# Kernel optimization log

Hardware: AMD Instinct MI355X
Metric: run time of the kernel (lower is better)

## Reference

```python
import jax, jax.numpy as jnp
import numpy as np
from jax.scipy.linalg import expm

B, S, D = 8, 2048, 1024          # batch, seq, input_dim
C, CD = 16, 64                   # num_concepts, concept_dim
L = C * CD                       # latent_dim = 1024
ALPHA, BETA = 0.3, 1.0
LN_EPS = 1e-5                    # torch nn.LayerNorm default


def layer_norm(x, g, b):
    m = jnp.mean(x, axis=-1, keepdims=True)
    v = jnp.mean(jnp.square(x - m), axis=-1, keepdims=True)
    return (x - m) * jax.lax.rsqrt(v + LN_EPS) * g + b


def setup_inputs() -> dict:
    key = jax.random.key(0)
    ks = jax.random.split(key, 8)
    sc = 0.02
    return {
        "x": jax.random.normal(ks[0], (B, S, D), jnp.float32),
        # encoder: Linear(D, 2L) + LayerNorm(2L)
        "enc_w": jax.random.normal(ks[1], (2 * L, D), jnp.float32) * sc,
        "enc_b": jnp.zeros((2 * L,), jnp.float32),
        "enc_g": jnp.ones((2 * L,), jnp.float32),
        "enc_bt": jnp.zeros((2 * L,), jnp.float32),
        # DAG weights [C, C] (torch inits zeros; use small random for non-trivial math)
        "dag_w": jax.random.normal(ks[2], (C, C), jnp.float32) * 0.1,
        # per-concept transforms: Linear(CD,CD) -> LN(CD) -> ReLU -> Linear(CD,CD), stacked over C
        "cw1": jax.random.normal(ks[3], (C, CD, CD), jnp.float32) * sc,
        "cb1": jnp.zeros((C, CD), jnp.float32),
        "cg": jnp.ones((C, CD), jnp.float32),
        "cbt": jnp.zeros((C, CD), jnp.float32),
        "cw2": jax.random.normal(ks[4], (C, CD, CD), jnp.float32) * sc,
        "cb2": jnp.zeros((C, CD), jnp.float32),
        # decoder: Linear(L,L) -> LN(L) -> ReLU -> Linear(L,D)
        "dec_w1": jax.random.normal(ks[5], (L, L), jnp.float32) * sc,
        "dec_b1": jnp.zeros((L,), jnp.float32),
        "dec_g": jnp.ones((L,), jnp.float32),
        "dec_bt": jnp.zeros((L,), jnp.float32),
        "dec_w2": jax.random.normal(ks[6], (D, L), jnp.float32) * sc,
        "dec_b2": jnp.zeros((D,), jnp.float32),
    }


def reference(x, enc_w, enc_b, enc_g, enc_bt, dag_w, cw1, cb1, cg, cbt, cw2, cb2,
              dec_w1, dec_b1, dec_g, dec_bt, dec_w2, dec_b2):
    # ---- encode ----
    h = layer_norm(jnp.einsum('bsd,kd->bsk', x, enc_w) + enc_b, enc_g, enc_bt)  # [B,S,2L]
    mu, logvar = jnp.split(h, 2, axis=-1)                                        # [B,S,L] each
    z = mu  # eval-mode reparameterize

    # ---- causal transform ----
    zc = z.reshape(B, S, C, CD)                                   # [B,S,C,CD]
    dag = jnp.tril(jax.nn.softplus(dag_w), k=-1)                  # [C,C]
    z_causal = zc + jnp.einsum('ij,bsjd->bsid', dag, zc)          # [B,S,C,CD]

    # per-concept Linear -> LN -> ReLU -> Linear, batched over concept axis
    t = jnp.einsum('bsce,cde->bscd', z_causal, cw1) + cb1         # [B,S,C,CD]
    t = layer_norm(t, cg, cbt)
    t = jax.nn.relu(t)
    t = jnp.einsum('bsce,cde->bscd', t, cw2) + cb2
    z_t = t.reshape(B, S, L)

    # ---- decode ----
    d = layer_norm(jnp.einsum('bsl,kl->bsk', z_t, dec_w1) + dec_b1, dec_g, dec_bt)
    d = jax.nn.relu(d)
    x_recon = jnp.einsum('bsl,dl->bsd', d, dec_w2) + dec_b2        # [B,S,D]

    # ---- losses ----
    recon_loss = jnp.mean(jnp.square(x_recon - x))
    kl_loss = -0.5 * jnp.mean(1.0 + logvar - jnp.square(mu) - jnp.exp(logvar))
    dag_loss = jnp.sum(jnp.abs(dag)) + jnp.trace(expm(dag))
    total_loss = recon_loss + ALPHA * kl_loss + BETA * dag_loss
    return x_recon, total_loss, kl_loss, recon_loss, dag_loss
```

## Files before the change

### kernel.cpp

```cpp
#include <hip/hip_runtime.h>
#include <stdint.h>


#define NTOK   16384
#define DIM    1024
#define NC     16
#define CD     64
#define NOUT_ELEMS 16777216

typedef float f32x4 __attribute__((ext_vector_type(4)));
typedef __bf16 bf16x8 __attribute__((ext_vector_type(8)));
typedef unsigned short u16x4 __attribute__((ext_vector_type(4)));
typedef unsigned short u16x8 __attribute__((ext_vector_type(8)));

__device__ float g_scal[3];
__device__ float g_part[512];

__device__ __forceinline__ float b2f(uint16_t u) {
  union { uint32_t i; float f; } v; v.i = ((uint32_t)u) << 16; return v.f;
}
__device__ __forceinline__ uint16_t f2b(float f) {
  union { float f; uint32_t i; } v; v.f = f;
  uint32_t x = v.i;
  return (uint16_t)((x + 0x7fffu + ((x >> 16) & 1u)) >> 16);
}

__device__ __forceinline__ void gload_lds16(const uint16_t* g, uint16_t* l) {
  __builtin_amdgcn_global_load_lds(
      (const __attribute__((address_space(1))) void*)g,
      (__attribute__((address_space(3))) void*)l, 16, 0, 0);
}

__device__ __forceinline__ void cvt8(const float* s, uint16_t* d) {
  const f32x4 a = *(const f32x4*)s;
  const f32x4 b = *(const f32x4*)(s + 4);
  u16x8 o;
  o[0]=f2b(a[0]); o[1]=f2b(a[1]); o[2]=f2b(a[2]); o[3]=f2b(a[3]);
  o[4]=f2b(b[0]); o[5]=f2b(b[1]); o[6]=f2b(b[2]); o[7]=f2b(b[3]);
  *(u16x8*)d = o;
}

__global__ __launch_bounds__(256) void cvt_all_kernel(
    const float* __restrict__ x, uint16_t* __restrict__ xdst,
    const float* __restrict__ ew, const float* __restrict__ d1,
    const float* __restrict__ d2, const float* __restrict__ c1,
    const float* __restrict__ c2, uint16_t* __restrict__ out,
    const float* __restrict__ dag_w)
{
  const int blk = blockIdx.x;
  if (blk < 8192) {
    const int i = blk * 256 + threadIdx.x;
    cvt8(x + (size_t)i * 8, xdst + (size_t)i * 8);
    return;
  }
  if (blk == 10304) {
    const int t = threadIdx.x;
    g_part[t] = 0.f;
    g_part[256 + t] = 0.f;
    const int i2 = t >> 4, j2 = t & 15;
    const float v = (j2 < i2) ? log1pf(expf(dag_w[t])) : 0.f;
    float s = v;
#pragma unroll
    for (int m = 1; m < 64; m <<= 1) s += __shfl_xor(s, m);
    __shared__ float red[4];
    const int wave = t >> 6, lane = t & 63;
    if (lane == 0) red[wave] = s;
    __syncthreads();
    if (t == 0)
      g_scal[2] = red[0] + red[1] + red[2] + red[3] + 16.f;
    return;
  }
  const int i = (blk - 8192) * 256 + threadIdx.x;
  const float* src; uint16_t* dst; int off;
  if (i < 262144)      { src = ew; dst = out;           off = i; }
  else if (i < 393216) { src = d1; dst = out + 2097152; off = i - 262144; }
  else if (i < 524288) { src = d2; dst = out + 3145728; off = i - 393216; }
  else if (i < 532480) { src = c1; dst = out + 4194304; off = i - 524288; }
  else                 { src = c2; dst = out + 4259840; off = i - 532480; }
  cvt8(src + (size_t)off * 8, dst + (size_t)off * 8);
}

__device__ __forceinline__ void stage_half(
    const uint16_t* __restrict__ G, uint16_t* L, int h, int lda,
    int sr, int pc, int wave)
{
#pragma unroll
  for (int i = 0; i < 2; ++i) {
    const int r = h * 128 + i * 64 + sr;
    gload_lds16(G + (size_t)r * lda + (size_t)((pc ^ (sr & 7)) * 8),
                (uint16_t*)((char*)L + h * 16384 + i * 8192 + wave * 1024));
  }
}

template<typename TC, bool SPLIT, int RECON_MODE>
__global__ __launch_bounds__(512, 2) void gemm256_kernel(
    const uint16_t* __restrict__ A, const uint16_t* __restrict__ Wm,
    const float* __restrict__ bias, TC* __restrict__ C0, TC* __restrict__ C1,
    const void* __restrict__ Xref,
    int K, int lda, int ldw, int ldc)
{
  __shared__ __align__(16) uint16_t lds[65536];

  const int tid  = threadIdx.x;
  const int wave = tid >> 6;
  const int lane = tid & 63;
  const int q    = lane >> 4;
  const int r16  = lane & 15;
  const int wm   = wave >> 2;
  const int wn   = wave & 3;
  const int sr   = tid >> 3;
  const int pc   = tid & 7;

  const int gx  = gridDim.x;
  const int gy  = gridDim.y;
  const int nwg = gx * gy;
  const int o   = blockIdx.y * gx + blockIdx.x;
  const int w   = (o & 7) * (nwg >> 3) + (o >> 3);
  const int bn  = (w & (gy - 1)) * 256;
  const int bm  = (w >> __builtin_ctz(gy)) * 256;

  const uint16_t* Ab = A  + (size_t)bm * lda;
  const uint16_t* Wb = Wm + (size_t)bn * ldw;

  const int T = K >> 6;

  stage_half(Ab,      lds,                 0, lda, sr, pc, wave);
  stage_half(Ab,      lds,                 1, lda, sr, pc, wave);
  stage_half(Wb,      lds + 16384,         0, ldw, sr, pc, wave);
  stage_half(Wb,      lds + 16384,         1, ldw, sr, pc, wave);
  if (T > 1) {
    stage_half(Wb + 64, lds + 32768 + 16384, 0, ldw, sr, pc, wave);
    stage_half(Wb + 64, lds + 32768 + 16384, 1, ldw, sr, pc, wave);
    asm volatile("s_waitcnt vmcnt(4)" ::: "memory");
  } else {
    asm volatile("s_waitcnt vmcnt(0)" ::: "memory");
  }
  __builtin_amdgcn_s_barrier();

  f32x4 acc[8][4] = {};
  const int cxa = r16 & 7;
  const int c0  = (q ^ cxa) * 8;
  const int c1  = ((4 + q) ^ cxa) * 8;

  for (int t = 0; t < T; ++t) {
    uint16_t* As  = lds + (t & 1) * 32768;
    uint16_t* Bs  = As + 16384;
    uint16_t* Asn = lds + ((t & 1) ^ 1) * 32768;

    const uint16_t* a_rd = As + (wm * 128 + r16) * 64;
    const uint16_t* b_rd = Bs + (wn * 64  + r16) * 64;

    bf16x8 bfr[4][2];

#pragma unroll
    for (int p = 0; p < 4; ++p) {
      bf16x8 af[2][2];
#pragma unroll
      for (int mi2 = 0; mi2 < 2; ++mi2) {
        af[mi2][0] = *(const bf16x8*)(a_rd + (p * 2 + mi2) * 1024 + c0);
        af[mi2][1] = *(const bf16x8*)(a_rd + (p * 2 + mi2) * 1024 + c1);
      }
      if (p == 0) {
#pragma unroll
        for (int ni = 0; ni < 4; ++ni) {
          bfr[ni][0] = *(const bf16x8*)(b_rd + ni * 1024 + c0);
          bfr[ni][1] = *(const bf16x8*)(b_rd + ni * 1024 + c1);
        }
        if (t + 1 < T) {
          stage_half(Ab + (size_t)(t + 1) * 64, Asn, 0, lda, sr, pc, wave);
          stage_half(Ab + (size_t)(t + 1) * 64, Asn, 1, lda, sr, pc, wave);
        }
      } else if (p == 1) {
        if (t + 2 < T)
          stage_half(Wb + (size_t)(t + 2) * 64, Bs, 0, ldw, sr, pc, wave);
      } else if (p == 2) {
        if (t + 2 < T)
          stage_half(Wb + (size_t)(t + 2) * 64, Bs, 1, ldw, sr, pc, wave);
      }

      __builtin_amdgcn_s_barrier();
      __builtin_amdgcn_s_setprio(1);
#pragma unroll
      for (int ks = 0; ks < 2; ++ks)
#pragma unroll
        for (int mi2 = 0; mi2 < 2; ++mi2)
#pragma unroll
          for (int ni = 0; ni < 4; ++ni)
            acc[p * 2 + mi2][ni] = __builtin_amdgcn_mfma_f32_16x16x32_bf16(
                af[mi2][ks], bfr[ni][ks], acc[p * 2 + mi2][ni], 0, 0, 0);
      __builtin_amdgcn_s_setprio(0);
      if (p == 3) {
        if (t + 2 < T)      asm volatile("s_waitcnt vmcnt(4)" ::: "memory");
        else if (t + 1 < T) asm volatile("s_waitcnt vmcnt(0)" ::: "memory");
      }
      __builtin_amdgcn_s_barrier();
    }
  }

  TC* Cq = C0;
  int cb = bn;
  if constexpr (SPLIT) {
    if (bn >= 1024) { Cq = C1; cb = bn - 1024; }
  }
  float bv[4];
#pragma unroll
  for (int ni = 0; ni < 4; ++ni) bv[ni] = bias[bn + wn * 64 + ni * 16 + r16];

  float rsum = 0.f;
#pragma unroll
  for (int mi = 0; mi < 8; ++mi) {
    const int rbase = bm + wm * 128 + mi * 16 + q * 4;
#pragma unroll
    for (int r = 0; r < 4; ++r) {
      const size_t rowoff = (size_t)(rbase + r) * ldc + cb;
#pragma unroll
      for (int ni = 0; ni < 4; ++ni) {
        const int loc = wn * 64 + ni * 16 + r16;
        const float v = acc[mi][ni][r] + bv[ni];
        if constexpr (sizeof(TC) == 2)
          Cq[rowoff + loc] = f2b(v);
        else
          Cq[rowoff + loc] = v;
        if constexpr (RECON_MODE == 1) {
          const float dd = v - ((const float*)Xref)[rowoff + loc];
          rsum += dd * dd;
        } else if constexpr (RECON_MODE == 2) {
          const float dd = v - b2f(((const uint16_t*)Xref)[rowoff + loc]);
          rsum += dd * dd;
        }
      }
    }
  }
  if constexpr (RECON_MODE != 0) {
#pragma unroll
    for (int m = 1; m < 64; m <<= 1) rsum += __shfl_xor(rsum, m);
    __shared__ float redR[8];
    if (lane == 0) redR[wave] = rsum;
    __syncthreads();
    if (tid == 0) {
      float s = 0.f;
#pragma unroll
      for (int w2 = 0; w2 < 8; ++w2) s += redR[w2];
      atomicAdd(&g_part[256 + (w & 255)], s);
    }
  }
}

__global__ __launch_bounds__(256) void concept_fused_kernel(
    uint16_t* __restrict__ z, const uint16_t* __restrict__ c1b,
    const uint16_t* __restrict__ c2b, const float* __restrict__ cb1,
    const float* __restrict__ cg, const float* __restrict__ cbt,
    const float* __restrict__ cb2)
{
  __shared__ __align__(16) uint16_t Az[128 * 64];
  __shared__ __align__(16) uint16_t W1s[64 * 64];
  __shared__ __align__(16) uint16_t W2s[64 * 64];

  const int tid  = threadIdx.x;
  const int wave = tid >> 6;
  const int lane = tid & 63;
  const int q    = lane >> 4;
  const int r16  = lane & 15;
  const int c    = blockIdx.y;
  const int m0   = blockIdx.x * 128;

  const int lr = tid >> 3;
  const int pc = tid & 7;

#pragma unroll
  for (int i = 0; i < 4; ++i) {
    const int r = i * 32 + lr;
    const int gc = pc ^ (r & 7);
    gload_lds16(z + (size_t)(m0 + r) * DIM + c * 64 + gc * 8,
                (uint16_t*)((char*)Az + i * 4096 + wave * 1024));
  }
#pragma unroll
  for (int i = 0; i < 2; ++i) {
    const int r = i * 32 + lr;
    const int gc = pc ^ (r & 7);
    gload_lds16(c1b + (size_t)c * 4096 + r * 64 + gc * 8,
                (uint16_t*)((char*)W1s + i * 4096 + wave * 1024));
    gload_lds16(c2b + (size_t)c * 4096 + r * 64 + gc * 8,
                (uint16_t*)((char*)W2s + i * 4096 + wave * 1024));
  }
  __syncthreads();

  f32x4 acc[2][4] = {};
#pragma unroll
  for (int ks = 0; ks < 2; ++ks) {
    bf16x8 af[2], wf[4];
#pragma unroll
    for (int mi = 0; mi < 2; ++mi) {
      const int row = wave * 32 + mi * 16 + r16;
      af[mi] = *(const bf16x8*)(Az + row * 64 + ((ks * 4 + q) ^ (row & 7)) * 8);
    }
#pragma unroll
    for (int ni = 0; ni < 4; ++ni) {
      const int d = ni * 16 + r16;
      wf[ni] = *(const bf16x8*)(W1s + d * 64 + ((ks * 4 + q) ^ (d & 7)) * 8);
    }
#pragma unroll
    for (int mi = 0; mi < 2; ++mi)
#pragma unroll
      for (int ni = 0; ni < 4; ++ni)
        acc[mi][ni] = __builtin_amdgcn_mfma_f32_16x16x32_bf16(
            af[mi], wf[ni], acc[mi][ni], 0, 0, 0);
  }

  float b1v[4], cgv[4], cbv[4], b2v[4];
#pragma unroll
  for (int ni = 0; ni < 4; ++ni) {
    const int cn = ni * 16 + r16;
    b1v[ni] = cb1[c * 64 + cn];
    cgv[ni] = cg[c * 64 + cn];
    cbv[ni] = cbt[c * 64 + cn];
    b2v[ni] = cb2[c * 64 + cn];
  }
#pragma unroll
  for (int mi = 0; mi < 2; ++mi) {
#pragma unroll
    for (int r = 0; r < 4; ++r) {
      float s1 = 0.f, s2 = 0.f;
#pragma unroll
      for (int ni = 0; ni < 4; ++ni) {
        const float v = acc[mi][ni][r] + b1v[ni];
        acc[mi][ni][r] = v;
        s1 += v; s2 += v * v;
      }
#pragma unroll
      for (int m = 1; m < 16; m <<= 1) {
        s1 += __shfl_xor(s1, m);
        s2 += __shfl_xor(s2, m);
      }
      const float mean = s1 * (1.f / 64.f);
      const float var  = s2 * (1.f / 64.f) - mean * mean;
      const float rs   = rsqrtf(var + 1e-5f);
      const int row = wave * 32 + mi * 16 + q * 4 + r;
#pragma unroll
      for (int ni = 0; ni < 4; ++ni) {
        const float y = fmaxf((acc[mi][ni][r] - mean) * rs * cgv[ni] + cbv[ni], 0.f);
        const int cn = ni * 16 + r16;
        Az[row * 64 + (((cn >> 3) ^ (row & 7)) * 8) + (cn & 7)] = f2b(y);
      }
    }
  }
  __syncthreads();

  f32x4 acc2[2][4] = {};
#pragma unroll
  for (int ks = 0; ks < 2; ++ks) {
    bf16x8 af[2], wf[4];
#pragma unroll
    for (int mi = 0; mi < 2; ++mi) {
      const int row = wave * 32 + mi * 16 + r16;
      af[mi] = *(const bf16x8*)(Az + row * 64 + ((ks * 4 + q) ^ (row & 7)) * 8);
    }
#pragma unroll
    for (int ni = 0; ni < 4; ++ni) {
      const int d = ni * 16 + r16;
      wf[ni] = *(const bf16x8*)(W2s + d * 64 + ((ks * 4 + q) ^ (d & 7)) * 8);
    }
#pragma unroll
    for (int mi = 0; mi < 2; ++mi)
#pragma unroll
      for (int ni = 0; ni < 4; ++ni)
        acc2[mi][ni] = __builtin_amdgcn_mfma_f32_16x16x32_bf16(
            af[mi], wf[ni], acc2[mi][ni], 0, 0, 0);
  }

#pragma unroll
  for (int mi = 0; mi < 2; ++mi)
#pragma unroll
    for (int ni = 0; ni < 4; ++ni) {
      const int cn = ni * 16 + r16;
#pragma unroll
      for (int r = 0; r < 4; ++r) {
        const int row = wave * 32 + mi * 16 + q * 4 + r;
        z[(size_t)(m0 + row) * DIM + c * 64 + cn] = f2b(acc2[mi][ni][r] + b2v[ni]);
      }
    }
}

__global__ __launch_bounds__(256) void kl_causal_kernel(
    const uint16_t* __restrict__ lv, uint16_t* __restrict__ mu,
    const float* __restrict__ g, const float* __restrict__ b,
    const float* __restrict__ dag_w)
{
  __shared__ __align__(16) float zsh[2][1024];
  __shared__ float dg[256];
  __shared__ float red[2][2][2];
  __shared__ float redk[2][2];
  const int tid  = threadIdx.x;
  const int tk   = tid >> 7;
  const int ttid = tid & 127;
  const int wv   = ttid >> 6;
  const int lane = tid & 63;
  const int tok  = blockIdx.x * 2 + tk;
  const int e0   = ttid * 8;

  dg[tid] = ((tid & 15) < (tid >> 4)) ? log1pf(expf(dag_w[tid])) : 0.f;

  const uint16_t* lvp = lv + (size_t)tok * 1024;
  uint16_t*       mup = mu + (size_t)tok * 1024;

  const u16x8 m8 = *(const u16x8*)(mup + e0);
  const u16x8 l8 = *(const u16x8*)(lvp + e0);
  float xm[8], xl[8];
  float s1 = 0.f, s2 = 0.f;
#pragma unroll
  for (int k = 0; k < 8; ++k) {
    xm[k] = b2f(m8[k]);
    xl[k] = b2f(l8[k]);
    s1 += xm[k] + xl[k];
    s2 += xm[k] * xm[k] + xl[k] * xl[k];
  }
#pragma unroll
  for (int m = 1; m < 64; m <<= 1) {
    s1 += __shfl_xor(s1, m);
    s2 += __shfl_xor(s2, m);
  }
  if (lane == 0) { red[tk][wv][0] = s1; red[tk][wv][1] = s2; }
  __syncthreads();
  s1 = red[tk][0][0] + red[tk][1][0];
  s2 = red[tk][0][1] + red[tk][1][1];
  const float mean = s1 * (1.f / 2048.f);
  const float var  = s2 * (1.f / 2048.f) - mean * mean;
  const float rs   = rsqrtf(var + 1e-5f);

  const f32x4 gm0 = *(const f32x4*)(g + e0);
  const f32x4 gm1 = *(const f32x4*)(g + e0 + 4);
  const f32x4 bm0 = *(const f32x4*)(b + e0);
  const f32x4 bm1 = *(const f32x4*)(b + e0 + 4);
  const f32x4 gl0 = *(const f32x4*)(g + 1024 + e0);
  const f32x4 gl1 = *(const f32x4*)(g + 1024 + e0 + 4);
  const f32x4 bl0 = *(const f32x4*)(b + 1024 + e0);
  const f32x4 bl1 = *(const f32x4*)(b + 1024 + e0 + 4);
  float kl = 0.f;
#pragma unroll
  for (int k = 0; k < 8; ++k) {
    const float gk = (k < 4) ? gm0[k] : gm1[k - 4];
    const float bk = (k < 4) ? bm0[k] : bm1[k - 4];
    const float glk = (k < 4) ? gl0[k] : gl1[k - 4];
    const float blk = (k < 4) ? bl0[k] : bl1[k - 4];
    const float zk = (xm[k] - mean) * rs * gk + bk;
    const float y  = (xl[k] - mean) * rs * glk + blk;
    kl += 1.f + y - zk * zk - expf(y);
    zsh[tk][e0 + k] = zk;
  }
#pragma unroll
  for (int m = 1; m < 64; m <<= 1) kl += __shfl_xor(kl, m);
  if (lane == 0) redk[tk][wv] = kl;
  __syncthreads();
  if (ttid == 0)
    atomicAdd(&g_part[tok & 255], redk[tk][0] + redk[tk][1]);

  const int i  = e0 >> 6;
  const int d0 = e0 & 63;
  f32x4 sa = *(const f32x4*)&zsh[tk][e0];
  f32x4 sb = *(const f32x4*)&zsh[tk][e0 + 4];
  for (int j = 0; j < i; ++j) {
    const float w = dg[i * 16 + j];
    const f32x4 za = *(const f32x4*)&zsh[tk][j * 64 + d0];
    const f32x4 zb = *(const f32x4*)&zsh[tk][j * 64 + d0 + 4];
#pragma unroll
    for (int k = 0; k < 4; ++k) { sa[k] += w * za[k]; sb[k] += w * zb[k]; }
  }
  u16x8 o;
#pragma unroll
  for (int k = 0; k < 4; ++k) { o[k] = f2b(sa[k]); o[4 + k] = f2b(sb[k]); }
  *(u16x8*)(mup + e0) = o;
}

__global__ __launch_bounds__(256) void ln_relu_kernel(
    uint16_t* __restrict__ data, const float* __restrict__ g,
    const float* __restrict__ b)
{
  __shared__ float red[2][2][2];
  const int tid  = threadIdx.x;
  const int tk   = tid >> 7;
  const int ttid = tid & 127;
  const int wv   = ttid >> 6;
  const int lane = tid & 63;
  const int e0   = ttid * 8;
  uint16_t* p = data + (size_t)(blockIdx.x * 2 + tk) * 1024;

  const u16x8 v8 = *(const u16x8*)(p + e0);
  float x[8];
  float s1 = 0.f, s2 = 0.f;
#pragma unroll
  for (int k = 0; k < 8; ++k) {
    x[k] = b2f(v8[k]);
    s1 += x[k];
    s2 += x[k] * x[k];
  }
#pragma unroll
  for (int m = 1; m < 64; m <<= 1) {
    s1 += __shfl_xor(s1, m);
    s2 += __shfl_xor(s2, m);
  }
  if (lane == 0) { red[tk][wv][0] = s1; red[tk][wv][1] = s2; }
  __syncthreads();
  s1 = red[tk][0][0] + red[tk][1][0];
  s2 = red[tk][0][1] + red[tk][1][1];
  const float mean = s1 * (1.f / 1024.f);
  const float var  = s2 * (1.f / 1024.f) - mean * mean;
  const float rs   = rsqrtf(var + 1e-5f);

  const f32x4 g0 = *(const f32x4*)(g + e0);
  const f32x4 g1 = *(const f32x4*)(g + e0 + 4);
  const f32x4 b0 = *(const f32x4*)(b + e0);
  const f32x4 b1 = *(const f32x4*)(b + e0 + 4);
  u16x8 o;
#pragma unroll
  for (int k = 0; k < 8; ++k) {
    const float gk = (k < 4) ? g0[k] : g1[k - 4];
    const float bk = (k < 4) ? b0[k] : b1[k - 4];
    o[k] = f2b(fmaxf((x[k] - mean) * rs * gk + bk, 0.f));
  }
  *(u16x8*)(p + e0) = o;
}

__global__ __launch_bounds__(256) void finalize_kernel(float* __restrict__ out_tail)
{
  const int tid = threadIdx.x;
  float kl = g_part[tid];
  float rc = g_part[256 + tid];
#pragma unroll
  for (int m = 1; m < 64; m <<= 1) {
    kl += __shfl_xor(kl, m);
    rc += __shfl_xor(rc, m);
  }
  __shared__ float red[8];
  const int wave = tid >> 6, lane = tid & 63;
  if (lane == 0) { red[wave] = kl; red[4 + wave] = rc; }
  __syncthreads();
  if (tid == 0) {
    const float kls = red[0] + red[1] + red[2] + red[3];
    const float rcs = red[4] + red[5] + red[6] + red[7];
    const float kl_l   = -0.5f * kls * (1.f / (16384.f * 1024.f));
    const float recon  = rcs * (1.f / 16777216.f);
    const float dagl   = g_scal[2];
    out_tail[0] = recon + 0.3f * kl_l + 1.0f * dagl;
    out_tail[1] = kl_l;
    out_tail[2] = recon;
    out_tail[3] = dagl;
  }
}

extern "C" void kernel_launch(void* const* d_in, const int* in_sizes, int n_in,
                              void* d_out, int out_size, void* d_ws, size_t ws_size,
                              hipStream_t stream) {
  const float* x      = (const float*)d_in[0];
  const float* enc_w  = (const float*)d_in[1];
  const float* enc_b  = (const float*)d_in[2];
  const float* enc_g  = (const float*)d_in[3];
  const float* enc_bt = (const float*)d_in[4];
  const float* dag_w  = (const float*)d_in[5];
  const float* cw1    = (const float*)d_in[6];
  const float* cb1    = (const float*)d_in[7];
  const float* cg     = (const float*)d_in[8];
  const float* cbt    = (const float*)d_in[9];
  const float* cw2    = (const float*)d_in[10];
  const float* cb2    = (const float*)d_in[11];
  const float* dec_w1 = (const float*)d_in[12];
  const float* dec_b1 = (const float*)d_in[13];
  const float* dec_g  = (const float*)d_in[14];
  const float* dec_bt = (const float*)d_in[15];
  const float* dec_w2 = (const float*)d_in[16];
  const float* dec_b2 = (const float*)d_in[17];

  uint16_t* S    = (uint16_t*)d_ws;
  uint16_t* Wbf  = (uint16_t*)((char*)d_ws + (size_t)NTOK * DIM * 2);
  uint16_t* ewb  = Wbf;
  uint16_t* d1b  = Wbf + 2097152;
  uint16_t* d2b  = Wbf + 3145728;
  uint16_t* c1b  = Wbf + 4194304;
  uint16_t* c2b  = Wbf + 4259840;

  uint16_t* Obf  = (uint16_t*)d_out;
  float*    O    = (float*)d_out;

  const size_t XBF2_OFF = (size_t)NTOK * DIM * 2 + (size_t)4325376 * 2;
  const bool ws_big = ws_size >= XBF2_OFF + (size_t)NTOK * DIM * 2;
  uint16_t* xbf = ws_big ? (uint16_t*)((char*)d_ws + XBF2_OFF)
                         : (uint16_t*)d_out + (size_t)NOUT_ELEMS;

  cvt_all_kernel<<<10305, 256, 0, stream>>>(
      x, xbf, enc_w, dec_w1, dec_w2, cw1, cw2, Wbf, dag_w);

  gemm256_kernel<uint16_t, true, 0>
      <<<dim3(64, 8, 1), 512, 0, stream>>>(
      xbf, ewb, enc_b, Obf, S, nullptr, DIM, DIM, DIM, DIM);

  kl_causal_kernel<<<NTOK / 2, 256, 0, stream>>>(S, Obf, enc_g, enc_bt, dag_w);

  concept_fused_kernel<<<dim3(128, 16, 1), 256, 0, stream>>>(
      Obf, c1b, c2b, cb1, cg, cbt, cb2);

  gemm256_kernel<uint16_t, false, 0>
      <<<dim3(64, 4, 1), 512, 0, stream>>>(
      Obf, d1b, dec_b1, S, S, nullptr, DIM, DIM, DIM, DIM);

  ln_relu_kernel<<<NTOK / 2, 256, 0, stream>>>(S, dec_g, dec_bt);

  if (ws_big) {
    gemm256_kernel<float, false, 2>
        <<<dim3(64, 4, 1), 512, 0, stream>>>(
        S, d2b, dec_b2, O, O, xbf, DIM, DIM, DIM, DIM);
  } else {
    gemm256_kernel<float, false, 1>
        <<<dim3(64, 4, 1), 512, 0, stream>>>(
        S, d2b, dec_b2, O, O, x, DIM, DIM, DIM, DIM);
  }

  finalize_kernel<<<1, 256, 0, stream>>>(O + (size_t)NOUT_ELEMS);
}
```

Baseline: 367.7 us.

## Fuse LN/KL/causal mix with per-concept MLP and fold finalize into last GEMM

Merges the encoder LayerNorm, KL accumulation and DAG causal mixing with the per-concept Linear-LN-ReLU-Linear MLP into one latent kernel. Each block handles 32 tokens and keeps the causal result in LDS, so the z round trip through global memory and one launch go away. The separate finalize kernel is replaced by a last-block-done counter in the final GEMM. In exchange, the per-concept weights are now read straight from global memory without swizzle, the grid is smaller (512 blocks), and the token loop is serialized with syncs.

```diff
diff --git a/kernel.cpp b/kernel.cpp
--- a/kernel.cpp
+++ b/kernel.cpp
@@ -15,6 +15,7 @@
 
 __device__ float g_scal[3];
 __device__ float g_part[512];
+__device__ int   g_ctr;
 
 __device__ __forceinline__ float b2f(uint16_t u) {
   union { uint32_t i; float f; } v; v.i = ((uint32_t)u) << 16; return v.f;
@@ -57,6 +58,7 @@
     const int t = threadIdx.x;
     g_part[t] = 0.f;
     g_part[256 + t] = 0.f;
+    if (t == 0) g_ctr = 0;
     const int i2 = t >> 4, j2 = t & 15;
     const float v = (j2 < i2) ? log1pf(expf(dag_w[t])) : 0.f;
     float s = v;
@@ -92,11 +94,11 @@
   }
 }
 
-template<typename TC, bool SPLIT, int RECON_MODE>
+template<typename TC, bool SPLIT, int RECON_MODE, bool FINAL>
 __global__ __launch_bounds__(512, 2) void gemm256_kernel(
     const uint16_t* __restrict__ A, const uint16_t* __restrict__ Wm,
     const float* __restrict__ bias, TC* __restrict__ C0, TC* __restrict__ C1,
-    const void* __restrict__ Xref,
+    const void* __restrict__ Xref, float* __restrict__ out_tail,
     int K, int lda, int ldw, int ldc)
 {
   __shared__ __align__(16) uint16_t lds[65536];
@@ -244,231 +246,249 @@
       atomicAdd(&g_part[256 + (w & 255)], s);
     }
   }
-}
-
-__global__ __launch_bounds__(256) void concept_fused_kernel(
-    uint16_t* __restrict__ z, const uint16_t* __restrict__ c1b,
-    const uint16_t* __restrict__ c2b, const float* __restrict__ cb1,
-    const float* __restrict__ cg, const float* __restrict__ cbt,
-    const float* __restrict__ cb2)
-{
-  __shared__ __align__(16) uint16_t Az[128 * 64];
-  __shared__ __align__(16) uint16_t W1s[64 * 64];
-  __shared__ __align__(16) uint16_t W2s[64 * 64];
-
-  const int tid  = threadIdx.x;
-  const int wave = tid >> 6;
-  const int lane = tid & 63;
-  const int q    = lane >> 4;
-  const int r16  = lane & 15;
-  const int c    = blockIdx.y;
-  const int m0   = blockIdx.x * 128;
-
-  const int lr = tid >> 3;
-  const int pc = tid & 7;
-
-#pragma unroll
-  for (int i = 0; i < 4; ++i) {
-    const int r = i * 32 + lr;
-    const int gc = pc ^ (r & 7);
-    gload_lds16(z + (size_t)(m0 + r) * DIM + c * 64 + gc * 8,
-                (uint16_t*)((char*)Az + i * 4096 + wave * 1024));
-  }
-#pragma unroll
-  for (int i = 0; i < 2; ++i) {
-    const int r = i * 32 + lr;
-    const int gc = pc ^ (r & 7);
-    gload_lds16(c1b + (size_t)c * 4096 + r * 64 + gc * 8,
-                (uint16_t*)((char*)W1s + i * 4096 + wave * 1024));
-    gload_lds16(c2b + (size_t)c * 4096 + r * 64 + gc * 8,
-                (uint16_t*)((char*)W2s + i * 4096 + wave * 1024));
-  }
-  __syncthreads();
-
-  f32x4 acc[2][4] = {};
-#pragma unroll
-  for (int ks = 0; ks < 2; ++ks) {
-    bf16x8 af[2], wf[4];
-#pragma unroll
-    for (int mi = 0; mi < 2; ++mi) {
-      const int row = wave * 32 + mi * 16 + r16;
-      af[mi] = *(const bf16x8*)(Az + row * 64 + ((ks * 4 + q) ^ (row & 7)) * 8);
-    }
-#pragma unroll
-    for (int ni = 0; ni < 4; ++ni) {
-      const int d = ni * 16 + r16;
-      wf[ni] = *(const bf16x8*)(W1s + d * 64 + ((ks * 4 + q) ^ (d & 7)) * 8);
-    }
-#pragma unroll
-    for (int mi = 0; mi < 2; ++mi)
-#pragma unroll
-      for (int ni = 0; ni < 4; ++ni)
-        acc[mi][ni] = __builtin_amdgcn_mfma_f32_16x16x32_bf16(
-            af[mi], wf[ni], acc[mi][ni], 0, 0, 0);
-  }
-
-  float b1v[4], cgv[4], cbv[4], b2v[4];
-#pragma unroll
-  for (int ni = 0; ni < 4; ++ni) {
-    const int cn = ni * 16 + r16;
-    b1v[ni] = cb1[c * 64 + cn];
-    cgv[ni] = cg[c * 64 + cn];
-    cbv[ni] = cbt[c * 64 + cn];
-    b2v[ni] = cb2[c * 64 + cn];
-  }
-#pragma unroll
-  for (int mi = 0; mi < 2; ++mi) {
-#pragma unroll
-    for (int r = 0; r < 4; ++r) {
-      float s1 = 0.f, s2 = 0.f;
-#pragma unroll
-      for (int ni = 0; ni < 4; ++ni) {
-        const float v = acc[mi][ni][r] + b1v[ni];
-        acc[mi][ni][r] = v;
-        s1 += v; s2 += v * v;
-      }
-#pragma unroll
-      for (int m = 1; m < 16; m <<= 1) {
-        s1 += __shfl_xor(s1, m);
-        s2 += __shfl_xor(s2, m);
-      }
-      const float mean = s1 * (1.f / 64.f);
-      const float var  = s2 * (1.f / 64.f) - mean * mean;
-      const float rs   = rsqrtf(var + 1e-5f);
-      const int row = wave * 32 + mi * 16 + q * 4 + r;
-#pragma unroll
-      for (int ni = 0; ni < 4; ++ni) {
-        const float y = fmaxf((acc[mi][ni][r] - mean) * rs * cgv[ni] + cbv[ni], 0.f);
-        const int cn = ni * 16 + r16;
-        Az[row * 64 + (((cn >> 3) ^ (row & 7)) * 8) + (cn & 7)] = f2b(y);
-      }
-    }
-  }
-  __syncthreads();
-
-  f32x4 acc2[2][4] = {};
-#pragma unroll
-  for (int ks = 0; ks < 2; ++ks) {
-    bf16x8 af[2], wf[4];
-#pragma unroll
-    for (int mi = 0; mi < 2; ++mi) {
-      const int row = wave * 32 + mi * 16 + r16;
-      af[mi] = *(const bf16x8*)(Az + row * 64 + ((ks * 4 + q) ^ (row & 7)) * 8);
-    }
-#pragma unroll
-    for (int ni = 0; ni < 4; ++ni) {
-      const int d = ni * 16 + r16;
-      wf[ni] = *(const bf16x8*)(W2s + d * 64 + ((ks * 4 + q) ^ (d & 7)) * 8);
-    }
-#pragma unroll
-    for (int mi = 0; mi < 2; ++mi)
-#pragma unroll
-      for (int ni = 0; ni < 4; ++ni)
-        acc2[mi][ni] = __builtin_amdgcn_mfma_f32_16x16x32_bf16(
-            af[mi], wf[ni], acc2[mi][ni], 0, 0, 0);
-  }
-
-#pragma unroll
-  for (int mi = 0; mi < 2; ++mi)
-#pragma unroll
-    for (int ni = 0; ni < 4; ++ni) {
-      const int cn = ni * 16 + r16;
-#pragma unroll
-      for (int r = 0; r < 4; ++r) {
-        const int row = wave * 32 + mi * 16 + q * 4 + r;
-        z[(size_t)(m0 + row) * DIM + c * 64 + cn] = f2b(acc2[mi][ni][r] + b2v[ni]);
-      }
-    }
-}
-
-__global__ __launch_bounds__(256) void kl_causal_kernel(
+  if constexpr (FINAL) {
+    __threadfence();
+    __shared__ int lastf;
+    if (tid == 0)
+      lastf = (atomicAdd(&g_ctr, 1) == (int)(gridDim.x * gridDim.y) - 1) ? 1 : 0;
+    __syncthreads();
+    if (lastf) {
+      float kl = 0.f, rc = 0.f;
+      if (tid < 256) {
+        kl = atomicAdd(&g_part[tid], 0.f);
+        rc = atomicAdd(&g_part[256 + tid], 0.f);
+      }
+#pragma unroll
+      for (int m = 1; m < 64; m <<= 1) {
+        kl += __shfl_xor(kl, m);
+        rc += __shfl_xor(rc, m);
+      }
+      __shared__ float redF[8];
+      if (lane == 0 && wave < 4) { redF[wave] = kl; redF[4 + wave] = rc; }
+      __syncthreads();
+      if (tid == 0) {
+        const float kls = redF[0] + redF[1] + redF[2] + redF[3];
+        const float rcs = redF[4] + redF[5] + redF[6] + redF[7];
+        const float kl_l  = -0.5f * kls * (1.f / (16384.f * 1024.f));
+        const float recon = rcs * (1.f / 16777216.f);
+        const float dagl  = g_scal[2];
+        out_tail[0] = recon + 0.3f * kl_l + 1.0f * dagl;
+        out_tail[1] = kl_l;
+        out_tail[2] = recon;
+        out_tail[3] = dagl;
+      }
+    }
+  }
+}
+
+__global__ __launch_bounds__(256) void latent_kernel(
     const uint16_t* __restrict__ lv, uint16_t* __restrict__ mu,
     const float* __restrict__ g, const float* __restrict__ b,
-    const float* __restrict__ dag_w)
+    const float* __restrict__ dag_w,
+    const uint16_t* __restrict__ c1b, const uint16_t* __restrict__ c2b,
+    const float* __restrict__ cb1, const float* __restrict__ cg,
+    const float* __restrict__ cbt, const float* __restrict__ cb2)
 {
+  __shared__ __align__(16) uint16_t Az[32 * 1024];
   __shared__ __align__(16) float zsh[2][1024];
   __shared__ float dg[256];
   __shared__ float red[2][2][2];
   __shared__ float redk[2][2];
+
   const int tid  = threadIdx.x;
   const int tk   = tid >> 7;
   const int ttid = tid & 127;
   const int wv   = ttid >> 6;
   const int lane = tid & 63;
-  const int tok  = blockIdx.x * 2 + tk;
   const int e0   = ttid * 8;
+  const int tok0 = blockIdx.x * 32;
 
   dg[tid] = ((tid & 15) < (tid >> 4)) ? log1pf(expf(dag_w[tid])) : 0.f;
 
-  const uint16_t* lvp = lv + (size_t)tok * 1024;
-  uint16_t*       mup = mu + (size_t)tok * 1024;
-
-  const u16x8 m8 = *(const u16x8*)(mup + e0);
-  const u16x8 l8 = *(const u16x8*)(lvp + e0);
-  float xm[8], xl[8];
-  float s1 = 0.f, s2 = 0.f;
-#pragma unroll
-  for (int k = 0; k < 8; ++k) {
-    xm[k] = b2f(m8[k]);
-    xl[k] = b2f(l8[k]);
-    s1 += xm[k] + xl[k];
-    s2 += xm[k] * xm[k] + xl[k] * xl[k];
-  }
-#pragma unroll
-  for (int m = 1; m < 64; m <<= 1) {
-    s1 += __shfl_xor(s1, m);
-    s2 += __shfl_xor(s2, m);
-  }
-  if (lane == 0) { red[tk][wv][0] = s1; red[tk][wv][1] = s2; }
-  __syncthreads();
-  s1 = red[tk][0][0] + red[tk][1][0];
-  s2 = red[tk][0][1] + red[tk][1][1];
-  const float mean = s1 * (1.f / 2048.f);
-  const float var  = s2 * (1.f / 2048.f) - mean * mean;
-  const float rs   = rsqrtf(var + 1e-5f);
-
-  const f32x4 gm0 = *(const f32x4*)(g + e0);
-  const f32x4 gm1 = *(const f32x4*)(g + e0 + 4);
-  const f32x4 bm0 = *(const f32x4*)(b + e0);
-  const f32x4 bm1 = *(const f32x4*)(b + e0 + 4);
-  const f32x4 gl0 = *(const f32x4*)(g + 1024 + e0);
-  const f32x4 gl1 = *(const f32x4*)(g + 1024 + e0 + 4);
-  const f32x4 bl0 = *(const f32x4*)(b + 1024 + e0);
-  const f32x4 bl1 = *(const f32x4*)(b + 1024 + e0 + 4);
-  float kl = 0.f;
-#pragma unroll
-  for (int k = 0; k < 8; ++k) {
-    const float gk = (k < 4) ? gm0[k] : gm1[k - 4];
-    const float bk = (k < 4) ? bm0[k] : bm1[k - 4];
-    const float glk = (k < 4) ? gl0[k] : gl1[k - 4];
-    const float blk = (k < 4) ? bl0[k] : bl1[k - 4];
-    const float zk = (xm[k] - mean) * rs * gk + bk;
-    const float y  = (xl[k] - mean) * rs * glk + blk;
-    kl += 1.f + y - zk * zk - expf(y);
-    zsh[tk][e0 + k] = zk;
-  }
-#pragma unroll
-  for (int m = 1; m < 64; m <<= 1) kl += __shfl_xor(kl, m);
-  if (lane == 0) redk[tk][wv] = kl;
-  __syncthreads();
-  if (ttid == 0)
-    atomicAdd(&g_part[tok & 255], redk[tk][0] + redk[tk][1]);
-
-  const int i  = e0 >> 6;
-  const int d0 = e0 & 63;
-  f32x4 sa = *(const f32x4*)&zsh[tk][e0];
-  f32x4 sb = *(const f32x4*)&zsh[tk][e0 + 4];
-  for (int j = 0; j < i; ++j) {
-    const float w = dg[i * 16 + j];
-    const f32x4 za = *(const f32x4*)&zsh[tk][j * 64 + d0];
-    const f32x4 zb = *(const f32x4*)&zsh[tk][j * 64 + d0 + 4];
-#pragma unroll
-    for (int k = 0; k < 4; ++k) { sa[k] += w * za[k]; sb[k] += w * zb[k]; }
-  }
-  u16x8 o;
-#pragma unroll
-  for (int k = 0; k < 4; ++k) { o[k] = f2b(sa[k]); o[4 + k] = f2b(sb[k]); }
-  *(u16x8*)(mup + e0) = o;
+  u16x8 m8 = *(const u16x8*)(mu + (size_t)(tok0 + tk) * 1024 + e0);
+  u16x8 l8 = *(const u16x8*)(lv + (size_t)(tok0 + tk) * 1024 + e0);
+
+  for (int pass = 0; pass < 16; ++pass) {
+    const int tok = tok0 + pass * 2 + tk;
+    float xm[8], xl[8];
+    float s1 = 0.f, s2 = 0.f;
+#pragma unroll
+    for (int k = 0; k < 8; ++k) {
+      xm[k] = b2f(m8[k]);
+      xl[k] = b2f(l8[k]);
+      s1 += xm[k] + xl[k];
+      s2 += xm[k] * xm[k] + xl[k] * xl[k];
+    }
+    if (pass < 15) {
+      m8 = *(const u16x8*)(mu + (size_t)(tok + 2) * 1024 + e0);
+      l8 = *(const u16x8*)(lv + (size_t)(tok + 2) * 1024 + e0);
+    }
+#pragma unroll
+    for (int m = 1; m < 64; m <<= 1) {
+      s1 += __shfl_xor(s1, m);
+      s2 += __shfl_xor(s2, m);
+    }
+    if (lane == 0) { red[tk][wv][0] = s1; red[tk][wv][1] = s2; }
+    __syncthreads();
+    s1 = red[tk][0][0] + red[tk][1][0];
+    s2 = red[tk][0][1] + red[tk][1][1];
+    const float mean = s1 * (1.f / 2048.f);
+    const float var  = s2 * (1.f / 2048.f) - mean * mean;
+    const float rs   = rsqrtf(var + 1e-5f);
+
+    const f32x4 gm0 = *(const f32x4*)(g + e0);
+    const f32x4 gm1 = *(const f32x4*)(g + e0 + 4);
+    const f32x4 bm0 = *(const f32x4*)(b + e0);
+    const f32x4 bm1 = *(const f32x4*)(b + e0 + 4);
+    const f32x4 gl0 = *(const f32x4*)(g + 1024 + e0);
+    const f32x4 gl1 = *(const f32x4*)(g + 1024 + e0 + 4);
+    const f32x4 bl0 = *(const f32x4*)(b + 1024 + e0);
+    const f32x4 bl1 = *(const f32x4*)(b + 1024 + e0 + 4);
+    float kl = 0.f;
+#pragma unroll
+    for (int k = 0; k < 8; ++k) {
+      const float gk  = (k < 4) ? gm0[k] : gm1[k - 4];
+      const float bk  = (k < 4) ? bm0[k] : bm1[k - 4];
+      const float glk = (k < 4) ? gl0[k] : gl1[k - 4];
+      const float blk = (k < 4) ? bl0[k] : bl1[k - 4];
+      const float zk = (xm[k] - mean) * rs * gk + bk;
+      const float y  = (xl[k] - mean) * rs * glk + blk;
+      kl += 1.f + y - zk * zk - expf(y);
+      zsh[tk][e0 + k] = zk;
+    }
+#pragma unroll
+    for (int m = 1; m < 64; m <<= 1) kl += __shfl_xor(kl, m);
+    if (lane == 0) redk[tk][wv] = kl;
+    __syncthreads();
+    if (ttid == 0)
+      atomicAdd(&g_part[tok & 255], redk[tk][0] + redk[tk][1]);
+
+    const int ci = e0 >> 6;
+    const int d0 = e0 & 63;
+    f32x4 sa = *(const f32x4*)&zsh[tk][e0];
+    f32x4 sb = *(const f32x4*)&zsh[tk][e0 + 4];
+    for (int j = 0; j < ci; ++j) {
+      const float wgt = dg[ci * 16 + j];
+      const f32x4 za = *(const f32x4*)&zsh[tk][j * 64 + d0];
+      const f32x4 zb = *(const f32x4*)&zsh[tk][j * 64 + d0 + 4];
+#pragma unroll
+      for (int k = 0; k < 4; ++k) { sa[k] += wgt * za[k]; sb[k] += wgt * zb[k]; }
+    }
+    const int row = pass * 2 + tk;
+    const int ch  = (e0 & 63) >> 3;
+    u16x8 o;
+#pragma unroll
+    for (int k = 0; k < 4; ++k) { o[k] = f2b(sa[k]); o[4 + k] = f2b(sb[k]); }
+    *(u16x8*)(Az + row * 1024 + ci * 64 + ((ch ^ (row & 7)) * 8)) = o;
+    __syncthreads();
+  }
+
+  const int q    = lane >> 4;
+  const int r16  = lane & 15;
+  const int wave = tid >> 6;
+
+  for (int cc = 0; cc < 4; ++cc) {
+    const int c = wave * 4 + cc;
+    const uint16_t* W1 = c1b + (size_t)c * 4096;
+    const uint16_t* W2 = c2b + (size_t)c * 4096;
+
+    f32x4 acc1[2][4] = {};
+#pragma unroll
+    for (int ks = 0; ks < 2; ++ks) {
+      bf16x8 af[2], wf[4];
+#pragma unroll
+      for (int mi = 0; mi < 2; ++mi) {
+        const int row = mi * 16 + r16;
+        af[mi] = *(const bf16x8*)(Az + row * 1024 + c * 64 +
+                                  (((ks * 4 + q) ^ (row & 7)) * 8));
+      }
+#pragma unroll
+      for (int ni = 0; ni < 4; ++ni) {
+        const int d = ni * 16 + r16;
+        wf[ni] = *(const bf16x8*)(W1 + d * 64 + (ks * 4 + q) * 8);
+      }
+#pragma unroll
+      for (int mi = 0; mi < 2; ++mi)
+#pragma unroll
+        for (int ni = 0; ni < 4; ++ni)
+          acc1[mi][ni] = __builtin_amdgcn_mfma_f32_16x16x32_bf16(
+              af[mi], wf[ni], acc1[mi][ni], 0, 0, 0);
+    }
+
+    float b1v[4], cgv[4], cbv[4], b2v[4];
+#pragma unroll
+    for (int ni = 0; ni < 4; ++ni) {
+      const int cn = ni * 16 + r16;
+      b1v[ni] = cb1[c * 64 + cn];
+      cgv[ni] = cg[c * 64 + cn];
+      cbv[ni] = cbt[c * 64 + cn];
+      b2v[ni] = cb2[c * 64 + cn];
+    }
+#pragma unroll
+    for (int mi = 0; mi < 2; ++mi) {
+#pragma unroll
+      for (int r = 0; r < 4; ++r) {
+        float s1 = 0.f, s2 = 0.f;
+#pragma unroll
+        for (int ni = 0; ni < 4; ++ni) {
+          const float v = acc1[mi][ni][r] + b1v[ni];
+          acc1[mi][ni][r] = v;
+          s1 += v; s2 += v * v;
+        }
+#pragma unroll
+        for (int m = 1; m < 16; m <<= 1) {
+          s1 += __shfl_xor(s1, m);
+          s2 += __shfl_xor(s2, m);
+        }
+        const float mean = s1 * (1.f / 64.f);
+        const float var  = s2 * (1.f / 64.f) - mean * mean;
+        const float rs   = rsqrtf(var + 1e-5f);
+        const int row = mi * 16 + q * 4 + r;
+#pragma unroll
+        for (int ni = 0; ni < 4; ++ni) {
+          const float y = fmaxf((acc1[mi][ni][r] - mean) * rs * cgv[ni] + cbv[ni], 0.f);
+          const int cn = ni * 16 + r16;
+          Az[row * 1024 + c * 64 + (((cn >> 3) ^ (row & 7)) * 8) + (cn & 7)] = f2b(y);
+        }
+      }
+    }
+    __syncthreads();
+
+    f32x4 acc2[2][4] = {};
+#pragma unroll
+    for (int ks = 0; ks < 2; ++ks) {
+      bf16x8 af[2], wf[4];
+#pragma unroll
+      for (int mi = 0; mi < 2; ++mi) {
+        const int row = mi * 16 + r16;
+        af[mi] = *(const bf16x8*)(Az + row * 1024 + c * 64 +
+                                  (((ks * 4 + q) ^ (row & 7)) * 8));
+      }
+#pragma unroll
+      for (int ni = 0; ni < 4; ++ni) {
+        const int d = ni * 16 + r16;
+        wf[ni] = *(const bf16x8*)(W2 + d * 64 + (ks * 4 + q) * 8);
+      }
+#pragma unroll
+      for (int mi = 0; mi < 2; ++mi)
+#pragma unroll
+        for (int ni = 0; ni < 4; ++ni)
+          acc2[mi][ni] = __builtin_amdgcn_mfma_f32_16x16x32_bf16(
+              af[mi], wf[ni], acc2[mi][ni], 0, 0, 0);
+    }
+
+#pragma unroll
+    for (int mi = 0; mi < 2; ++mi)
+#pragma unroll
+      for (int ni = 0; ni < 4; ++ni) {
+        const int cn = ni * 16 + r16;
+#pragma unroll
+        for (int r = 0; r < 4; ++r) {
+          const int row = mi * 16 + q * 4 + r;
+          mu[(size_t)(tok0 + row) * 1024 + c * 64 + cn] = f2b(acc2[mi][ni][r] + b2v[ni]);
+        }
+      }
+  }
 }
 
 __global__ __launch_bounds__(256) void ln_relu_kernel(
@@ -518,33 +538,6 @@
     o[k] = f2b(fmaxf((x[k] - mean) * rs * gk + bk, 0.f));
   }
   *(u16x8*)(p + e0) = o;
-}
-
-__global__ __launch_bounds__(256) void finalize_kernel(float* __restrict__ out_tail)
-{
-  const int tid = threadIdx.x;
-  float kl = g_part[tid];
-  float rc = g_part[256 + tid];
-#pragma unroll
-  for (int m = 1; m < 64; m <<= 1) {
-    kl += __shfl_xor(kl, m);
-    rc += __shfl_xor(rc, m);
-  }
-  __shared__ float red[8];
-  const int wave = tid >> 6, lane = tid & 63;
-  if (lane == 0) { red[wave] = kl; red[4 + wave] = rc; }
-  __syncthreads();
-  if (tid == 0) {
-    const float kls = red[0] + red[1] + red[2] + red[3];
-    const float rcs = red[4] + red[5] + red[6] + red[7];
-    const float kl_l   = -0.5f * kls * (1.f / (16384.f * 1024.f));
-    const float recon  = rcs * (1.f / 16777216.f);
-    const float dagl   = g_scal[2];
-    out_tail[0] = recon + 0.3f * kl_l + 1.0f * dagl;
-    out_tail[1] = kl_l;
-    out_tail[2] = recon;
-    out_tail[3] = dagl;
-  }
 }
 
 extern "C" void kernel_launch(void* const* d_in, const int* in_sizes, int n_in,
@@ -588,30 +581,26 @@
   cvt_all_kernel<<<10305, 256, 0, stream>>>(
       x, xbf, enc_w, dec_w1, dec_w2, cw1, cw2, Wbf, dag_w);
 
-  gemm256_kernel<uint16_t, true, 0>
+  gemm256_kernel<uint16_t, true, 0, false>
       <<<dim3(64, 8, 1), 512, 0, stream>>>(
-      xbf, ewb, enc_b, Obf, S, nullptr, DIM, DIM, DIM, DIM);
-
-  kl_causal_kernel<<<NTOK / 2, 256, 0, stream>>>(S, Obf, enc_g, enc_bt, dag_w);
-
-  concept_fused_kernel<<<dim3(128, 16, 1), 256, 0, stream>>>(
-      Obf, c1b, c2b, cb1, cg, cbt, cb2);
-
-  gemm256_kernel<uint16_t, false, 0>
+      xbf, ewb, enc_b, Obf, S, nullptr, nullptr, DIM, DIM, DIM, DIM);
+
+  latent_kernel<<<NTOK / 32, 256, 0, stream>>>(
+      S, Obf, enc_g, enc_bt, dag_w, c1b, c2b, cb1, cg, cbt, cb2);
+
+  gemm256_kernel<uint16_t, false, 0, false>
       <<<dim3(64, 4, 1), 512, 0, stream>>>(
-      Obf, d1b, dec_b1, S, S, nullptr, DIM, DIM, DIM, DIM);
+      Obf, d1b, dec_b1, S, S, nullptr, nullptr, DIM, DIM, DIM, DIM);
 
   ln_relu_kernel<<<NTOK / 2, 256, 0, stream>>>(S, dec_g, dec_bt);
 
   if (ws_big) {
-    gemm256_kernel<float, false, 2>
+    gemm256_kernel<float, false, 2, true>
         <<<dim3(64, 4, 1), 512, 0, stream>>>(
-        S, d2b, dec_b2, O, O, xbf, DIM, DIM, DIM, DIM);
+        S, d2b, dec_b2, O, O, xbf, O + (size_t)NOUT_ELEMS, DIM, DIM, DIM, DIM);
   } else {
-    gemm256_kernel<float, false, 1>
+    gemm256_kernel<float, false, 1, true>
         <<<dim3(64, 4, 1), 512, 0, stream>>>(
-        S, d2b, dec_b2, O, O, x, DIM, DIM, DIM, DIM);
-  }
-
-  finalize_kernel<<<1, 256, 0, stream>>>(O + (size_t)NOUT_ELEMS);
-}
+        S, d2b, dec_b2, O, O, x, O + (size_t)NOUT_ELEMS, DIM, DIM, DIM, DIM);
+  }
+}
```

Measured after the change: 433.0 us. +17.7%, slower.
